# Kernel optimization log

Measured on AMD Instinct MI355X. Metric: run time of the kernel, lower is better.

## Reference

```python
import jax, jax.numpy as jnp
import numpy as np

B, T = 32, 512
DA, DV = 1280, 768
D = DA + DV          # fused audio+video feature dim = 2048
DM = 256             # mamba d_model
L = 4                # n_layers
DI = 2 * DM          # d_inner (expand=2)
DS = 16              # d_state
DC = 4               # d_conv
R = DM // 16         # dt_rank = ceil(256/16)
H = 128              # attn-pool hidden
NC = 8               # emotion classes
EPS_TIN = 1e-5
EPS_LN = 1e-5


def _ln(x, g, b):
    mu = x.mean(-1, keepdims=True)
    v = ((x - mu) ** 2).mean(-1, keepdims=True)
    return (x - mu) / jnp.sqrt(v + EPS_LN) * g + b


def _mamba(u, in_w, cw, cb, xw, dtw, dtb, A_log, Dp, ow):
    # u: [B,T,DM] -> [B,T,DM]; Mamba(v1) selective scan, d_state=16, d_conv=4, expand=2
    xz = jnp.einsum('btd,ed->bte', u, in_w)            # [B,T,2*DI]
    x, z = xz[..., :DI], xz[..., DI:]
    xp = jnp.pad(x, ((0, 0), (DC - 1, 0), (0, 0)))     # causal depthwise conv1d
    xc = sum(xp[:, k:k + u.shape[1], :] * cw[:, k] for k in range(DC)) + cb
    x = jax.nn.silu(xc)
    dbc = jnp.einsum('btd,ed->bte', x, xw)             # [B,T,R+2*DS]
    dt = jax.nn.softplus(jnp.einsum('btr,dr->btd', dbc[..., :R], dtw) + dtb)
    Bm = dbc[..., R:R + DS]
    Cm = dbc[..., R + DS:]
    A = -jnp.exp(A_log)                                # [DI,DS]

    def step(h, inp):
        dt_t, B_t, C_t, x_t = inp                      # [B,DI],[B,DS],[B,DS],[B,DI]
        h = jnp.exp(dt_t[..., None] * A) * h + dt_t[..., None] * B_t[:, None, :] * x_t[..., None]
        return h, jnp.einsum('bds,bs->bd', h, C_t)

    h0 = jnp.zeros((u.shape[0], DI, DS), u.dtype)
    xs = (dt.swapaxes(0, 1), Bm.swapaxes(0, 1), Cm.swapaxes(0, 1), x.swapaxes(0, 1))
    _, ys = jax.lax.scan(step, h0, xs)
    y = ys.swapaxes(0, 1) + Dp * x
    y = y * jax.nn.silu(z)
    return jnp.einsum('bti,oi->bto', y, ow)


def _forward(x, tin_gamma, tin_beta, proj_w, proj_b, ln_g, ln_b, in_proj_w, conv_w, conv_b,
             x_proj_w, dt_proj_w, dt_proj_b, A_log, D_param, out_proj_w,
             out_ln_g, out_ln_b, res_scale, attn_w1, attn_b1, attn_w2, head_w, head_b, lengths):
    mask = jnp.arange(T)[None, :] < lengths[:, None]   # [B,T]
    m = mask[..., None].astype(x.dtype)
    # FusedTIN: masked temporal instance norm + affine
    denom = jnp.maximum(lengths, 1).astype(x.dtype)[:, None, None]
    mean = (x * m).sum(1, keepdims=True) / denom
    var = (((x - mean) ** 2) * m).sum(1, keepdims=True) / denom
    xn = (x - mean) / jnp.sqrt(var + EPS_TIN) * m
    xn = (xn * tin_gamma + tin_beta) * m
    # MambaStack: proj_in + prenorm residual mamba blocks (dropout = eval identity)
    h = jnp.einsum('btd,md->btm', xn, proj_w) + proj_b
    for l in range(L):
        y = _mamba(_ln(h, ln_g[l], ln_b[l]), in_proj_w[l], conv_w[l], conv_b[l],
                   x_proj_w[l], dt_proj_w[l], dt_proj_b[l], A_log[l], D_param[l], out_proj_w[l])
        h = h + res_scale * y
    h = _ln(h, out_ln_g, out_ln_b)
    # MaskedAttnPool
    s = jnp.einsum('bth,oh->bto', jnp.tanh(jnp.einsum('btd,hd->bth', h, attn_w1) + attn_b1), attn_w2)[..., 0]
    logits = jnp.where(mask, s, -jnp.inf)
    alpha = jnp.nan_to_num(jax.nn.softmax(logits, axis=1)) * mask
    alpha = alpha / jnp.clip(alpha.sum(1, keepdims=True), 1e-9)
    ctx = (alpha[..., None] * h).sum(1)
    # classifier head
    return jnp.einsum('bd,cd->bc', ctx, head_w) + head_b


def setup_inputs() -> dict:
    key = jax.random.key(0)
    ks = jax.random.split(key, 16)
    s = 0.05
    inp = {}
    inp['x'] = jax.random.normal(ks[0], (B, T, D), jnp.float32)
    inp['lengths'] = jax.random.randint(ks[1], (B,), T // 4, T + 1)
    inp['tin_gamma'] = jnp.ones((D,), jnp.float32)
    inp['tin_beta'] = jnp.zeros((D,), jnp.float32)
    inp['proj_w'] = jax.random.normal(ks[2], (DM, D), jnp.float32) * s
    inp['proj_b'] = jnp.zeros((DM,), jnp.float32)
    inp['ln_g'] = jnp.ones((L, DM), jnp.float32)
    inp['ln_b'] = jnp.zeros((L, DM), jnp.float32)
    inp['in_proj_w'] = jax.random.normal(ks[3], (L, 2 * DI, DM), jnp.float32) * s
    inp['conv_w'] = jax.random.normal(ks[4], (L, DI, DC), jnp.float32) * s
    inp['conv_b'] = jnp.zeros((L, DI), jnp.float32)
    inp['x_proj_w'] = jax.random.normal(ks[5], (L, R + 2 * DS, DI), jnp.float32) * s
    inp['dt_proj_w'] = jax.random.normal(ks[6], (L, DI, R), jnp.float32) * s
    inp['dt_proj_b'] = jnp.full((L, DI), -3.0, jnp.float32) + jax.random.normal(ks[7], (L, DI), jnp.float32) * 0.1
    inp['A_log'] = jnp.log(jnp.broadcast_to(jnp.arange(1, DS + 1, dtype=jnp.float32), (L, DI, DS)) + 0.0)
    inp['D_param'] = jnp.ones((L, DI), jnp.float32)
    inp['out_proj_w'] = jax.random.normal(ks[8], (L, DM, DI), jnp.float32) * s
    inp['out_ln_g'] = jnp.ones((DM,), jnp.float32)
    inp['out_ln_b'] = jnp.zeros((DM,), jnp.float32)
    inp['res_scale'] = jnp.asarray(0.1, jnp.float32)
    inp['attn_w1'] = jax.random.normal(ks[9], (H, DM), jnp.float32) * s
    inp['attn_b1'] = jnp.zeros((H,), jnp.float32)
    inp['attn_w2'] = jax.random.normal(ks[10], (1, H), jnp.float32) * s
    inp['head_w'] = jax.random.normal(ks[11], (NC, DM), jnp.float32) * s
    inp['head_b'] = jnp.zeros((NC,), jnp.float32)
    return inp


def reference(x, tin_gamma, tin_beta, proj_w, proj_b, ln_g, ln_b, in_proj_w, conv_w, conv_b,
              x_proj_w, dt_proj_w, dt_proj_b, A_log, D_param, out_proj_w,
              out_ln_g, out_ln_b, res_scale, attn_w1, attn_b1, attn_w2, head_w, head_b, lengths):
    return _forward(x, tin_gamma, tin_beta, proj_w, proj_b, ln_g, ln_b, in_proj_w, conv_w, conv_b,
                    x_proj_w, dt_proj_w, dt_proj_b, A_log, D_param, out_proj_w,
                    out_ln_g, out_ln_b, res_scale, attn_w1, attn_b1, attn_w2, head_w, head_b, lengths)
```

## Files before the change

kernel.cpp:

```cpp
#include <hip/hip_runtime.h>

#define NB 32
#define NT 512
#define ND 2048
#define NDM 256
#define NDI 512
#define NDS 16
#define NR 16
#define NDC 4
#define NH 128
#define NNC 8
#define NL 4
#define NM (NB*NT)

typedef __attribute__((ext_vector_type(8))) short short8;
typedef __attribute__((ext_vector_type(4))) float floatx4;

__device__ __forceinline__ unsigned short f2bf_rn(float f) {
    unsigned u = __builtin_bit_cast(unsigned, f);
    u += 0x7FFFu + ((u >> 16) & 1u);
    return (unsigned short)(u >> 16);
}

__global__ __launch_bounds__(256) void tin_stats_k(
    const float* __restrict__ x, const int* __restrict__ lengths,
    float* __restrict__ mean, float* __restrict__ rstd)
{
    __shared__ float rs_[4][64];
    __shared__ float rq_[4][64];
    const int b = blockIdx.x >> 5;
    const int d0 = (blockIdx.x & 31) << 6;
    const int dl = threadIdx.x & 63;
    const int strip = threadIdx.x >> 6;
    const int len = lengths[b];
    const int d = d0 + dl;
    float s = 0.f, q = 0.f;
    for (int t = strip; t < len; t += 4) {
        float v = x[((size_t)(b*NT + t))*ND + d];
        s += v; q += v*v;
    }
    rs_[strip][dl] = s; rq_[strip][dl] = q;
    __syncthreads();
    if (threadIdx.x < 64) {
        float S = rs_[0][dl]+rs_[1][dl]+rs_[2][dl]+rs_[3][dl];
        float Q = rq_[0][dl]+rq_[1][dl]+rq_[2][dl]+rq_[3][dl];
        float inv = 1.f / (float)(len < 1 ? 1 : len);
        float mu = S * inv;
        float var = Q * inv - mu*mu;
        mean[b*ND + d] = mu;
        rstd[b*ND + d] = rsqrtf(var + 1e-5f);
    }
}

#define A_HI 0
#define A_LO 4096
#define B_HI 8192
#define B_LO 12288

template<int AMODE, int EPI>
__global__ __launch_bounds__(256) void mgemm_k(
    const float* __restrict__ A, int lda,
    const float* __restrict__ A2, int lda2,
    const float* __restrict__ W,
    const float* __restrict__ bias,
    float* __restrict__ C,
    int M, int N, int K,
    const float* __restrict__ mean, const float* __restrict__ rstd,
    const float* __restrict__ gamma, const float* __restrict__ beta,
    const int* __restrict__ lengths,
    const float* __restrict__ rsp)
{
    __shared__ __align__(16) short lds[16384];
    const int tid = threadIdx.x;
    const int lane = tid & 63;
    const int w = tid >> 6;
    const int lm = lane & 15;
    const int lc = lane >> 4;
    const int wm = w >> 1;
    const int wn = w & 1;
    const int m0 = blockIdx.x * 128;
    const int n0 = blockIdx.y * 128;

    int lenb = 0, bb = 0;
    if (AMODE == 1) { bb = m0 >> 9; lenb = lengths[bb]; }

    floatx4 acc[4][4];
#pragma unroll
    for (int i = 0; i < 4; ++i)
#pragma unroll
        for (int j = 0; j < 4; ++j) acc[i][j] = (floatx4){0.f,0.f,0.f,0.f};

    for (int k0 = 0; k0 < K; k0 += 32) {
        float va[2][8], vb[2][8];
#pragma unroll
        for (int hh = 0; hh < 2; ++hh) {
            const int mt = w*2 + hh;
            const int gm = m0 + mt*16 + lm;
            const int kg = k0 + lc*8;
            const float* ap = A + (size_t)gm*lda + kg;
            float4 a0 = *(const float4*)ap;
            float4 a1 = *(const float4*)(ap + 4);
            if (AMODE == 1) {
                const int tcur = gm & (NT-1);
                if (tcur >= lenb) {
                    a0 = make_float4(0.f,0.f,0.f,0.f); a1 = a0;
                } else {
                    const int kb = bb*ND + kg;
                    float4 mn0 = *(const float4*)(mean + kb);
                    float4 mn1 = *(const float4*)(mean + kb + 4);
                    float4 rr0 = *(const float4*)(rstd + kb);
                    float4 rr1 = *(const float4*)(rstd + kb + 4);
                    float4 g0 = *(const float4*)(gamma + kg);
                    float4 g1 = *(const float4*)(gamma + kg + 4);
                    float4 e0 = *(const float4*)(beta + kg);
                    float4 e1 = *(const float4*)(beta + kg + 4);
                    a0.x = (a0.x - mn0.x)*rr0.x*g0.x + e0.x;
                    a0.y = (a0.y - mn0.y)*rr0.y*g0.y + e0.y;
                    a0.z = (a0.z - mn0.z)*rr0.z*g0.z + e0.z;
                    a0.w = (a0.w - mn0.w)*rr0.w*g0.w + e0.w;
                    a1.x = (a1.x - mn1.x)*rr1.x*g1.x + e1.x;
                    a1.y = (a1.y - mn1.y)*rr1.y*g1.y + e1.y;
                    a1.z = (a1.z - mn1.z)*rr1.z*g1.z + e1.z;
                    a1.w = (a1.w - mn1.w)*rr1.w*g1.w + e1.w;
                }
            } else if (AMODE == 2) {
                const float* zp = A2 + (size_t)gm*lda2 + kg;
                float4 z0 = *(const float4*)zp;
                float4 z1 = *(const float4*)(zp + 4);
                a0.x *= z0.x / (1.f + __expf(-z0.x));
                a0.y *= z0.y / (1.f + __expf(-z0.y));
                a0.z *= z0.z / (1.f + __expf(-z0.z));
                a0.w *= z0.w / (1.f + __expf(-z0.w));
                a1.x *= z1.x / (1.f + __expf(-z1.x));
                a1.y *= z1.y / (1.f + __expf(-z1.y));
                a1.z *= z1.z / (1.f + __expf(-z1.z));
                a1.w *= z1.w / (1.f + __expf(-z1.w));
            }
            va[hh][0]=a0.x; va[hh][1]=a0.y; va[hh][2]=a0.z; va[hh][3]=a0.w;
            va[hh][4]=a1.x; va[hh][5]=a1.y; va[hh][6]=a1.z; va[hh][7]=a1.w;
        }
#pragma unroll
        for (int hh = 0; hh < 2; ++hh) {
            const int nt = w*2 + hh;
            const int gn = n0 + nt*16 + lm;
            float4 w0, w1;
            if (gn < N) {
                const float* wp = W + (size_t)gn*K + k0 + lc*8;
                w0 = *(const float4*)wp;
                w1 = *(const float4*)(wp + 4);
            } else {
                w0 = make_float4(0.f,0.f,0.f,0.f); w1 = w0;
            }
            vb[hh][0]=w0.x; vb[hh][1]=w0.y; vb[hh][2]=w0.z; vb[hh][3]=w0.w;
            vb[hh][4]=w1.x; vb[hh][5]=w1.y; vb[hh][6]=w1.z; vb[hh][7]=w1.w;
        }
        __syncthreads();
#pragma unroll
        for (int hh = 0; hh < 2; ++hh) {
            short8 h8, l8;
#pragma unroll
            for (int q = 0; q < 8; ++q) {
                unsigned short hb = f2bf_rn(va[hh][q]);
                float hf = __builtin_bit_cast(float, (unsigned)hb << 16);
                h8[q] = (short)hb;
                l8[q] = (short)f2bf_rn(va[hh][q] - hf);
            }
            const int off = ((w*2 + hh)*64 + lane)*8;
            *(short8*)&lds[A_HI + off] = h8;
            *(short8*)&lds[A_LO + off] = l8;
        }
#pragma unroll
        for (int hh = 0; hh < 2; ++hh) {
            short8 h8, l8;
#pragma unroll
            for (int q = 0; q < 8; ++q) {
                unsigned short hb = f2bf_rn(vb[hh][q]);
                float hf = __builtin_bit_cast(float, (unsigned)hb << 16);
                h8[q] = (short)hb;
                l8[q] = (short)f2bf_rn(vb[hh][q] - hf);
            }
            const int off = ((w*2 + hh)*64 + lane)*8;
            *(short8*)&lds[B_HI + off] = h8;
            *(short8*)&lds[B_LO + off] = l8;
        }
        __syncthreads();
        short8 ah[4], al[4], bh[4], bl[4];
#pragma unroll
        for (int i = 0; i < 4; ++i) {
            const int off = ((wm*4 + i)*64 + lane)*8;
            ah[i] = *(const short8*)&lds[A_HI + off];
            al[i] = *(const short8*)&lds[A_LO + off];
        }
#pragma unroll
        for (int j = 0; j < 4; ++j) {
            const int off = ((wn*4 + j)*64 + lane)*8;
            bh[j] = *(const short8*)&lds[B_HI + off];
            bl[j] = *(const short8*)&lds[B_LO + off];
        }
#pragma unroll
        for (int i = 0; i < 4; ++i)
#pragma unroll
            for (int j = 0; j < 4; ++j) {
                acc[i][j] = __builtin_amdgcn_mfma_f32_16x16x32_bf16(ah[i], bh[j], acc[i][j], 0, 0, 0);
                acc[i][j] = __builtin_amdgcn_mfma_f32_16x16x32_bf16(ah[i], bl[j], acc[i][j], 0, 0, 0);
                acc[i][j] = __builtin_amdgcn_mfma_f32_16x16x32_bf16(al[i], bh[j], acc[i][j], 0, 0, 0);
            }
    }

    const float rs = (EPI == 1) ? rsp[0] : 0.f;
#pragma unroll
    for (int j = 0; j < 4; ++j) {
        const int n = n0 + wn*64 + j*16 + lm;
        if (n < N) {
            const float bv = (EPI != 1 && bias) ? bias[n] : 0.f;
#pragma unroll
            for (int i = 0; i < 4; ++i) {
#pragma unroll
                for (int r = 0; r < 4; ++r) {
                    const int m = m0 + wm*64 + i*16 + lc*4 + r;
                    float v = acc[i][j][r];
                    float* cp = C + (size_t)m*N + n;
                    if (EPI == 0)      *cp = v + bv;
                    else if (EPI == 1) *cp = fmaf(rs, v, *cp);
                    else               *cp = tanhf(v + bv);
                }
            }
        }
    }
}

__global__ __launch_bounds__(256) void ln_k(
    const float* __restrict__ in, float* __restrict__ out,
    const float* __restrict__ g, const float* __restrict__ b)
{
    const int w = threadIdx.x >> 6;
    const int lane = threadIdx.x & 63;
    const int m = blockIdx.x*4 + w;
    const float4 v = *(const float4*)(in + (size_t)m*NDM + lane*4);
    float s = v.x+v.y+v.z+v.w;
    float q = v.x*v.x + v.y*v.y + v.z*v.z + v.w*v.w;
#pragma unroll
    for (int o = 32; o; o >>= 1) { s += __shfl_xor(s, o); q += __shfl_xor(q, o); }
    const float mu = s * (1.f/NDM);
    const float var = q * (1.f/NDM) - mu*mu;
    const float r = rsqrtf(var + 1e-5f);
    const float4 g4 = *(const float4*)(g + lane*4);
    const float4 b4 = *(const float4*)(b + lane*4);
    float4 o;
    o.x = (v.x-mu)*r*g4.x + b4.x;
    o.y = (v.y-mu)*r*g4.y + b4.y;
    o.z = (v.z-mu)*r*g4.z + b4.z;
    o.w = (v.w-mu)*r*g4.w + b4.w;
    *(float4*)(out + (size_t)m*NDM + lane*4) = o;
}

__global__ __launch_bounds__(256) void conv_k(
    const float* __restrict__ xz, const float* __restrict__ cw,
    const float* __restrict__ cb, float* __restrict__ xc)
{
    const int m = blockIdx.x >> 1;
    const int i = ((blockIdx.x & 1) << 8) + threadIdx.x;
    const int t = m & (NT-1);
    const float4 w4 = *(const float4*)(cw + i*4);
    const float* base = xz + (size_t)m*(2*NDI) + i;
    float acc = cb[i] + base[0]*w4.w;
    if (t >= 1) acc += base[-(2*NDI)]  * w4.z;
    if (t >= 2) acc += base[-2*(2*NDI)]* w4.y;
    if (t >= 3) acc += base[-3*(2*NDI)]* w4.x;
    xc[(size_t)m*NDI + i] = acc / (1.f + __expf(-acc));
}

#define TCH 64
__global__ __launch_bounds__(256) void scan_k(
    const float* __restrict__ dbc,
    const float* __restrict__ xc,
    const float* __restrict__ dtw,
    const float* __restrict__ dtb,
    const float* __restrict__ Alog,
    const float* __restrict__ Dp,
    float* __restrict__ y)
{
    __shared__ float sR[TCH][16];
    __shared__ float sB[TCH][16];
    __shared__ float sC[TCH][16];
    __shared__ float sX[TCH][16];
    __shared__ float sDT[TCH][16];
    __shared__ float sY[TCH][16];
    const int tid = threadIdx.x;
    const int s = tid & 15;
    const int di = tid >> 4;
    const int b = blockIdx.x >> 5;
    const int d0 = (blockIdx.x & 31) << 4;
    const int d = d0 + di;
    const float Av = -__expf(Alog[d*NDS + s]);
    const float dpv = Dp[d];
    const float dtbd = dtb[d];
    float wrow[16];
#pragma unroll
    for (int r = 0; r < 16; ++r) wrow[r] = dtw[d*NR + r];
    float h = 0.f;
    const int jrow = tid >> 2;
    const int q4 = (tid & 3) << 2;
    const size_t mbase = (size_t)b * NT;
    for (int c0 = 0; c0 < NT; c0 += TCH) {
        __syncthreads();
        {
            const size_t m = mbase + c0 + jrow;
            const float* dp_ = dbc + m*48 + q4;
            *(float4*)&sR[jrow][q4] = *(const float4*)(dp_);
            *(float4*)&sB[jrow][q4] = *(const float4*)(dp_ + 16);
            *(float4*)&sC[jrow][q4] = *(const float4*)(dp_ + 32);
            *(float4*)&sX[jrow][q4] = *(const float4*)(xc + m*NDI + d0 + q4);
        }
        __syncthreads();
#pragma unroll
        for (int u2 = 0; u2 < 4; ++u2) {
            const int j = s + u2*16;
            float a = dtbd;
#pragma unroll
            for (int r = 0; r < 16; ++r) a = fmaf(sR[j][r], wrow[r], a);
            sDT[j][di] = (a > 20.f) ? a : log1pf(__expf(a));
        }
        __syncthreads();
        for (int j = 0; j < TCH; ++j) {
            const float dtv = sDT[j][di];
            const float xv = sX[j][di];
            const float Bv = sB[j][s];
            const float Cv = sC[j][s];
            const float pa = __expf(dtv * Av);
            h = fmaf(pa, h, dtv * Bv * xv);
            float cp = h * Cv;
            cp += __shfl_xor(cp, 1);
            cp += __shfl_xor(cp, 2);
            cp += __shfl_xor(cp, 4);
            cp += __shfl_xor(cp, 8);
            if (s == 0) sY[j][di] = fmaf(dpv, xv, cp);
        }
        __syncthreads();
        {
            const size_t m = mbase + c0 + jrow;
            *(float4*)(y + m*NDI + d0 + q4) = *(const float4*)&sY[jrow][q4];
        }
    }
}

__global__ __launch_bounds__(64) void score_k(
    const float* __restrict__ t1, const float* __restrict__ w2,
    float* __restrict__ sout)
{
    const int m = blockIdx.x;
    const int lane = threadIdx.x;
    float v = t1[(size_t)m*NH + lane]*w2[lane]
            + t1[(size_t)m*NH + 64 + lane]*w2[64 + lane];
#pragma unroll
    for (int o = 32; o; o >>= 1) v += __shfl_xor(v, o);
    if (lane == 0) sout[m] = v;
}

__global__ __launch_bounds__(256) void pool_k(
    const float* __restrict__ sbuf, const float* __restrict__ u,
    const int* __restrict__ lengths, float* __restrict__ ctx)
{
    __shared__ float al[NT];
    __shared__ float red[256];
    const int b = blockIdx.x;
    const int tid = threadIdx.x;
    const int len = lengths[b];
    float mx = -3.4e38f;
    for (int t = tid; t < len; t += 256) mx = fmaxf(mx, sbuf[b*NT + t]);
    red[tid] = mx; __syncthreads();
    for (int o = 128; o; o >>= 1) { if (tid < o) red[tid] = fmaxf(red[tid], red[tid+o]); __syncthreads(); }
    mx = red[0];
    __syncthreads();
    float sm = 0.f;
    for (int t = tid; t < len; t += 256) {
        float e = __expf(sbuf[b*NT + t] - mx);
        al[t] = e; sm += e;
    }
    red[tid] = sm; __syncthreads();
    for (int o = 128; o; o >>= 1) { if (tid < o) red[tid] += red[tid+o]; __syncthreads(); }
    const float rZ = 1.f / red[0];
    float acc = 0.f;
    const float* up = u + (size_t)b*NT*NDM + tid;
    for (int t = 0; t < len; ++t) acc = fmaf(al[t], up[(size_t)t*NDM], acc);
    ctx[b*NDM + tid] = acc * rZ;
}

__global__ __launch_bounds__(64) void head_k(
    const float* __restrict__ ctx, const float* __restrict__ hw,
    const float* __restrict__ hb, float* __restrict__ o)
{
    const int b = blockIdx.x;
    const int lane = threadIdx.x;
    const float4 c4 = *(const float4*)(ctx + b*NDM + lane*4);
#pragma unroll
    for (int c = 0; c < NNC; ++c) {
        const float4 w4 = *(const float4*)(hw + c*NDM + lane*4);
        float v = c4.x*w4.x + c4.y*w4.y + c4.z*w4.z + c4.w*w4.w;
#pragma unroll
        for (int off = 32; off; off >>= 1) v += __shfl_xor(v, off);
        if (lane == 0) o[b*NNC + c] = v + hb[c];
    }
}

extern "C" void kernel_launch(void* const* d_in, const int* in_sizes, int n_in,
                              void* d_out, int out_size, void* d_ws, size_t ws_size,
                              hipStream_t stream)
{
    (void)in_sizes; (void)n_in; (void)out_size; (void)ws_size;
    const float* x         = (const float*)d_in[0];
    const int*   lengths   = (const int*)  d_in[1];
    const float* tin_gamma = (const float*)d_in[2];
    const float* tin_beta  = (const float*)d_in[3];
    const float* proj_w    = (const float*)d_in[4];
    const float* proj_b    = (const float*)d_in[5];
    const float* ln_g      = (const float*)d_in[6];
    const float* ln_b      = (const float*)d_in[7];
    const float* in_proj_w = (const float*)d_in[8];
    const float* conv_w    = (const float*)d_in[9];
    const float* conv_b    = (const float*)d_in[10];
    const float* x_proj_w  = (const float*)d_in[11];
    const float* dt_proj_w = (const float*)d_in[12];
    const float* dt_proj_b = (const float*)d_in[13];
    const float* A_log     = (const float*)d_in[14];
    const float* D_param   = (const float*)d_in[15];
    const float* out_proj_w= (const float*)d_in[16];
    const float* out_ln_g  = (const float*)d_in[17];
    const float* out_ln_b  = (const float*)d_in[18];
    const float* res_scale = (const float*)d_in[19];
    const float* attn_w1   = (const float*)d_in[20];
    const float* attn_b1   = (const float*)d_in[21];
    const float* attn_w2   = (const float*)d_in[22];
    const float* head_w    = (const float*)d_in[23];
    const float* head_b    = (const float*)d_in[24];
    float* out = (float*)d_out;

    float* ws   = (float*)d_ws;
    float* mean = ws;
    float* rstd = mean + (size_t)NB*ND;
    float* hbuf = rstd + (size_t)NB*ND;
    float* ubuf = hbuf + (size_t)NM*NDM;
    float* xz   = ubuf + (size_t)NM*NDM;
    float* xc   = xz   + (size_t)NM*2*NDI;
    float* ybuf = xc   + (size_t)NM*NDI;
    float* dbc  = ybuf + (size_t)NM*NDI;
    float* t1   = dbc  + (size_t)NM*48;
    float* sbuf = t1   + (size_t)NM*NH;
    float* ctx  = sbuf + NM;

    const dim3 blk(256);

    tin_stats_k<<<dim3(NB*32), blk, 0, stream>>>(x, lengths, mean, rstd);
    mgemm_k<1,0><<<dim3(NM/128, NDM/128), blk, 0, stream>>>(
        x, ND, nullptr, 0, proj_w, proj_b, hbuf, NM, NDM, ND,
        mean, rstd, tin_gamma, tin_beta, lengths, nullptr);

    for (int l = 0; l < NL; ++l) {
        ln_k<<<dim3(NM/4), blk, 0, stream>>>(hbuf, ubuf, ln_g + l*NDM, ln_b + l*NDM);
        mgemm_k<0,0><<<dim3(NM/128, (2*NDI)/128), blk, 0, stream>>>(
            ubuf, NDM, nullptr, 0, in_proj_w + (size_t)l*2*NDI*NDM, nullptr,
            xz, NM, 2*NDI, NDM, nullptr, nullptr, nullptr, nullptr, nullptr, nullptr);
        conv_k<<<dim3(NM*2), blk, 0, stream>>>(
            xz, conv_w + (size_t)l*NDI*NDC, conv_b + (size_t)l*NDI, xc);
        mgemm_k<0,0><<<dim3(NM/128, 1), blk, 0, stream>>>(
            xc, NDI, nullptr, 0, x_proj_w + (size_t)l*48*NDI, nullptr,
            dbc, NM, 48, NDI, nullptr, nullptr, nullptr, nullptr, nullptr, nullptr);
        scan_k<<<dim3(NB*32), blk, 0, stream>>>(
            dbc, xc, dt_proj_w + (size_t)l*NDI*NR, dt_proj_b + (size_t)l*NDI,
            A_log + (size_t)l*NDI*NDS, D_param + (size_t)l*NDI, ybuf);
        mgemm_k<2,1><<<dim3(NM/128, NDM/128), blk, 0, stream>>>(
            ybuf, NDI, xz + NDI, 2*NDI, out_proj_w + (size_t)l*NDM*NDI, nullptr,
            hbuf, NM, NDM, NDI, nullptr, nullptr, nullptr, nullptr, nullptr, res_scale);
    }

    ln_k<<<dim3(NM/4), blk, 0, stream>>>(hbuf, ubuf, out_ln_g, out_ln_b);
    mgemm_k<0,2><<<dim3(NM/128, 1), blk, 0, stream>>>(
        ubuf, NDM, nullptr, 0, attn_w1, attn_b1, t1, NM, NH, NDM,
        nullptr, nullptr, nullptr, nullptr, nullptr, nullptr);
    score_k<<<dim3(NM), dim3(64), 0, stream>>>(t1, attn_w2, sbuf);
    pool_k<<<dim3(NB), blk, 0, stream>>>(sbuf, ubuf, lengths, ctx);
    head_k<<<dim3(NB), dim3(64), 0, stream>>>(ctx, head_w, head_b, out);
}
```

Baseline: 1.865 ms.

## Pre-split operands into blocked bf16 hi/lo tiles and restructure Mamba pipeline

Producers (TIN norm, layernorm, conv, scan) now write activations directly as pre-split bf16 hi/lo pairs in an MFMA-fragment-blocked layout, and weights are converted once per call by a new wconv kernel. The GEMM becomes a templated kernel with configurable tile sizes that streams pre-converted fragments with register prefetch instead of doing fp32 loads and conversion inside the K loop. The dt projection is split out into its own kernel, the scan is reworked to cover more channels per block and fuse the SiLU(z) gating plus hi/lo conversion, and conv and layernorm are blocked to match. This removes repeated fp32-to-bf16 splitting and fused prologue math from the GEMM inner loops. In exchange it adds extra kernels, extra intermediate buffers and more memory traffic for the split activations.

```diff
diff --git a/kernel.cpp b/kernel.cpp
--- a/kernel.cpp
+++ b/kernel.cpp
@@ -7,7 +7,6 @@
 #define NDI 512
 #define NDS 16
 #define NR 16
-#define NDC 4
 #define NH 128
 #define NNC 8
 #define NL 4
@@ -20,6 +19,15 @@
     unsigned u = __builtin_bit_cast(unsigned, f);
     u += 0x7FFFu + ((u >> 16) & 1u);
     return (unsigned short)(u >> 16);
+}
+__device__ __forceinline__ void cvt8(const float* v, short8& h8, short8& l8) {
+#pragma unroll
+    for (int q = 0; q < 8; ++q) {
+        unsigned short hb = f2bf_rn(v[q]);
+        float hf = __builtin_bit_cast(float, (unsigned)hb << 16);
+        h8[q] = (short)hb;
+        l8[q] = (short)f2bf_rn(v[q] - hf);
+    }
 }
 
 __global__ __launch_bounds__(256) void tin_stats_k(
@@ -52,174 +60,189 @@
     }
 }
 
-#define A_HI 0
-#define A_LO 4096
-#define B_HI 8192
-#define B_LO 12288
-
-template<int AMODE, int EPI>
+#define SLN 264
+__global__ __launch_bounds__(256) void tin_norm_k(
+    const float* __restrict__ x, const int* __restrict__ lengths,
+    const float* __restrict__ mean, const float* __restrict__ rstd,
+    const float* __restrict__ g, const float* __restrict__ be,
+    short* __restrict__ Oh, short* __restrict__ Ol)
+{
+    __shared__ float sT[16][SLN];
+    const int tid = threadIdx.x;
+    const int row = tid >> 4, c = tid & 15;
+    const int m = blockIdx.x*16 + row;
+    const int b = m >> 9, t = m & (NT-1);
+    const int len = lengths[b];
+    const int kg0 = blockIdx.y*256 + c*16;
+    if (t >= len) {
+#pragma unroll
+        for (int i = 0; i < 16; ++i) sT[row][c*16 + i] = 0.f;
+    } else {
+#pragma unroll
+        for (int qq = 0; qq < 4; ++qq) {
+            const int kg = kg0 + qq*4;
+            float4 v = *(const float4*)(x + (size_t)m*ND + kg);
+            float4 mn = *(const float4*)(mean + b*ND + kg);
+            float4 rr = *(const float4*)(rstd + b*ND + kg);
+            float4 gg = *(const float4*)(g + kg);
+            float4 bb = *(const float4*)(be + kg);
+            sT[row][c*16+qq*4+0] = (v.x-mn.x)*rr.x*gg.x + bb.x;
+            sT[row][c*16+qq*4+1] = (v.y-mn.y)*rr.y*gg.y + bb.y;
+            sT[row][c*16+qq*4+2] = (v.z-mn.z)*rr.z*gg.z + bb.z;
+            sT[row][c*16+qq*4+3] = (v.w-mn.w)*rr.w*gg.w + bb.w;
+        }
+    }
+    __syncthreads();
+#pragma unroll
+    for (int q = 0; q < 2; ++q) {
+        const int slot = tid + 256*q;
+        const int tile = slot >> 6, ln2 = slot & 63;
+        const int mr = ln2 & 15, kc = ln2 >> 4;
+        float v[8];
+        *(float4*)&v[0] = *(const float4*)&sT[mr][tile*32 + kc*8];
+        *(float4*)&v[4] = *(const float4*)&sT[mr][tile*32 + kc*8 + 4];
+        short8 h8, l8; cvt8(v, h8, l8);
+        const size_t off = ((size_t)blockIdx.x*64 + blockIdx.y*8 + tile)*512 + ln2*8;
+        *(short8*)(Oh + off) = h8;
+        *(short8*)(Ol + off) = l8;
+    }
+}
+
+__global__ __launch_bounds__(256) void wconv_k(
+    const float* __restrict__ W, short* __restrict__ Oh, short* __restrict__ Ol,
+    int K, int nmod, int nvalid)
+{
+    __shared__ float sT[16][SLN];
+    const int tid = threadIdx.x;
+    const int row = tid >> 4, c = tid & 15;
+    const int n = blockIdx.x*16 + row;
+    const int rr = n % nmod;
+    const int kg0 = blockIdx.y*256 + c*16;
+    if (rr >= nvalid) {
+#pragma unroll
+        for (int i = 0; i < 16; ++i) sT[row][c*16 + i] = 0.f;
+    } else {
+        const int src = (n/nmod)*nvalid + rr;
+#pragma unroll
+        for (int qq = 0; qq < 4; ++qq) {
+            float4 v = *(const float4*)(W + (size_t)src*K + kg0 + qq*4);
+            *(float4*)&sT[row][c*16+qq*4] = v;
+        }
+    }
+    __syncthreads();
+#pragma unroll
+    for (int q = 0; q < 2; ++q) {
+        const int slot = tid + 256*q;
+        const int tile = slot >> 6, ln2 = slot & 63;
+        const int mr = ln2 & 15, kc = ln2 >> 4;
+        float v[8];
+        *(float4*)&v[0] = *(const float4*)&sT[mr][tile*32 + kc*8];
+        *(float4*)&v[4] = *(const float4*)&sT[mr][tile*32 + kc*8 + 4];
+        short8 h8, l8; cvt8(v, h8, l8);
+        const size_t off = ((size_t)blockIdx.x*(K>>5) + blockIdx.y*8 + tile)*512 + ln2*8;
+        *(short8*)(Oh + off) = h8;
+        *(short8*)(Ol + off) = l8;
+    }
+}
+
+template<int MSUB, int NSUB, int EPI>
 __global__ __launch_bounds__(256) void mgemm_k(
-    const float* __restrict__ A, int lda,
-    const float* __restrict__ A2, int lda2,
-    const float* __restrict__ W,
-    const float* __restrict__ bias,
-    float* __restrict__ C,
-    int M, int N, int K,
-    const float* __restrict__ mean, const float* __restrict__ rstd,
-    const float* __restrict__ gamma, const float* __restrict__ beta,
-    const int* __restrict__ lengths,
-    const float* __restrict__ rsp)
-{
-    __shared__ __align__(16) short lds[16384];
-    const int tid = threadIdx.x;
-    const int lane = tid & 63;
-    const int w = tid >> 6;
-    const int lm = lane & 15;
-    const int lc = lane >> 4;
-    const int wm = w >> 1;
-    const int wn = w & 1;
-    const int m0 = blockIdx.x * 128;
-    const int n0 = blockIdx.y * 128;
-
-    int lenb = 0, bb = 0;
-    if (AMODE == 1) { bb = m0 >> 9; lenb = lengths[bb]; }
-
-    floatx4 acc[4][4];
-#pragma unroll
-    for (int i = 0; i < 4; ++i)
-#pragma unroll
-        for (int j = 0; j < 4; ++j) acc[i][j] = (floatx4){0.f,0.f,0.f,0.f};
-
-    for (int k0 = 0; k0 < K; k0 += 32) {
-        float va[2][8], vb[2][8];
-#pragma unroll
-        for (int hh = 0; hh < 2; ++hh) {
-            const int mt = w*2 + hh;
-            const int gm = m0 + mt*16 + lm;
-            const int kg = k0 + lc*8;
-            const float* ap = A + (size_t)gm*lda + kg;
-            float4 a0 = *(const float4*)ap;
-            float4 a1 = *(const float4*)(ap + 4);
-            if (AMODE == 1) {
-                const int tcur = gm & (NT-1);
-                if (tcur >= lenb) {
-                    a0 = make_float4(0.f,0.f,0.f,0.f); a1 = a0;
-                } else {
-                    const int kb = bb*ND + kg;
-                    float4 mn0 = *(const float4*)(mean + kb);
-                    float4 mn1 = *(const float4*)(mean + kb + 4);
-                    float4 rr0 = *(const float4*)(rstd + kb);
-                    float4 rr1 = *(const float4*)(rstd + kb + 4);
-                    float4 g0 = *(const float4*)(gamma + kg);
-                    float4 g1 = *(const float4*)(gamma + kg + 4);
-                    float4 e0 = *(const float4*)(beta + kg);
-                    float4 e1 = *(const float4*)(beta + kg + 4);
-                    a0.x = (a0.x - mn0.x)*rr0.x*g0.x + e0.x;
-                    a0.y = (a0.y - mn0.y)*rr0.y*g0.y + e0.y;
-                    a0.z = (a0.z - mn0.z)*rr0.z*g0.z + e0.z;
-                    a0.w = (a0.w - mn0.w)*rr0.w*g0.w + e0.w;
-                    a1.x = (a1.x - mn1.x)*rr1.x*g1.x + e1.x;
-                    a1.y = (a1.y - mn1.y)*rr1.y*g1.y + e1.y;
-                    a1.z = (a1.z - mn1.z)*rr1.z*g1.z + e1.z;
-                    a1.w = (a1.w - mn1.w)*rr1.w*g1.w + e1.w;
-                }
-            } else if (AMODE == 2) {
-                const float* zp = A2 + (size_t)gm*lda2 + kg;
-                float4 z0 = *(const float4*)zp;
-                float4 z1 = *(const float4*)(zp + 4);
-                a0.x *= z0.x / (1.f + __expf(-z0.x));
-                a0.y *= z0.y / (1.f + __expf(-z0.y));
-                a0.z *= z0.z / (1.f + __expf(-z0.z));
-                a0.w *= z0.w / (1.f + __expf(-z0.w));
-                a1.x *= z1.x / (1.f + __expf(-z1.x));
-                a1.y *= z1.y / (1.f + __expf(-z1.y));
-                a1.z *= z1.z / (1.f + __expf(-z1.z));
-                a1.w *= z1.w / (1.f + __expf(-z1.w));
+    const short* __restrict__ Ah, const short* __restrict__ Al,
+    const short* __restrict__ Bh, const short* __restrict__ Bl,
+    const float* __restrict__ bias, float* __restrict__ C,
+    int ldc, int Nvalid, int K, const float* __restrict__ rsp)
+{
+    __shared__ __align__(16) short lds[(MSUB+NSUB)*1024];
+    short* As_h = lds;
+    short* As_l = lds + MSUB*512;
+    short* Bs_h = lds + MSUB*1024;
+    short* Bs_l = lds + MSUB*1024 + NSUB*512;
+    const int tid = threadIdx.x, lane = tid & 63, w = tid >> 6;
+    const int m0t = blockIdx.x * MSUB;
+    const int n0t = blockIdx.y * NSUB;
+    const int Ktiles = K >> 5;
+    constexpr int MI = MSUB/2, NI = NSUB/2;
+    constexpr int ASG = MSUB/4, BSG = NSUB/4;
+    const int wm = w >> 1, wn = w & 1;
+
+    floatx4 acc[MI][NI] = {};
+    short8 rah[ASG], ral[ASG], rbh[BSG], rbl[BSG];
+
+#pragma unroll
+    for (int u = 0; u < ASG; ++u) {
+        const size_t off = ((size_t)(m0t + w*ASG + u)*Ktiles)*512 + lane*8;
+        rah[u] = *(const short8*)(Ah + off); ral[u] = *(const short8*)(Al + off);
+    }
+#pragma unroll
+    for (int u = 0; u < BSG; ++u) {
+        const size_t off = ((size_t)(n0t + w*BSG + u)*Ktiles)*512 + lane*8;
+        rbh[u] = *(const short8*)(Bh + off); rbl[u] = *(const short8*)(Bl + off);
+    }
+
+    for (int kb = 0; kb < Ktiles; ++kb) {
+        __syncthreads();
+#pragma unroll
+        for (int u = 0; u < ASG; ++u) {
+            const int sub = w*ASG + u;
+            *(short8*)&As_h[sub*512 + lane*8] = rah[u];
+            *(short8*)&As_l[sub*512 + lane*8] = ral[u];
+        }
+#pragma unroll
+        for (int u = 0; u < BSG; ++u) {
+            const int sub = w*BSG + u;
+            *(short8*)&Bs_h[sub*512 + lane*8] = rbh[u];
+            *(short8*)&Bs_l[sub*512 + lane*8] = rbl[u];
+        }
+        __syncthreads();
+        if (kb + 1 < Ktiles) {
+#pragma unroll
+            for (int u = 0; u < ASG; ++u) {
+                const size_t off = ((size_t)(m0t + w*ASG + u)*Ktiles + kb + 1)*512 + lane*8;
+                rah[u] = *(const short8*)(Ah + off); ral[u] = *(const short8*)(Al + off);
             }
-            va[hh][0]=a0.x; va[hh][1]=a0.y; va[hh][2]=a0.z; va[hh][3]=a0.w;
-            va[hh][4]=a1.x; va[hh][5]=a1.y; va[hh][6]=a1.z; va[hh][7]=a1.w;
-        }
-#pragma unroll
-        for (int hh = 0; hh < 2; ++hh) {
-            const int nt = w*2 + hh;
-            const int gn = n0 + nt*16 + lm;
-            float4 w0, w1;
-            if (gn < N) {
-                const float* wp = W + (size_t)gn*K + k0 + lc*8;
-                w0 = *(const float4*)wp;
-                w1 = *(const float4*)(wp + 4);
-            } else {
-                w0 = make_float4(0.f,0.f,0.f,0.f); w1 = w0;
+#pragma unroll
+            for (int u = 0; u < BSG; ++u) {
+                const size_t off = ((size_t)(n0t + w*BSG + u)*Ktiles + kb + 1)*512 + lane*8;
+                rbh[u] = *(const short8*)(Bh + off); rbl[u] = *(const short8*)(Bl + off);
             }
-            vb[hh][0]=w0.x; vb[hh][1]=w0.y; vb[hh][2]=w0.z; vb[hh][3]=w0.w;
-            vb[hh][4]=w1.x; vb[hh][5]=w1.y; vb[hh][6]=w1.z; vb[hh][7]=w1.w;
-        }
-        __syncthreads();
-#pragma unroll
-        for (int hh = 0; hh < 2; ++hh) {
-            short8 h8, l8;
-#pragma unroll
-            for (int q = 0; q < 8; ++q) {
-                unsigned short hb = f2bf_rn(va[hh][q]);
-                float hf = __builtin_bit_cast(float, (unsigned)hb << 16);
-                h8[q] = (short)hb;
-                l8[q] = (short)f2bf_rn(va[hh][q] - hf);
+        }
+        short8 fah[MI], fal[MI], fbh[NI], fbl[NI];
+#pragma unroll
+        for (int i = 0; i < MI; ++i) {
+            const int sub = wm*MI + i;
+            fah[i] = *(const short8*)&As_h[sub*512 + lane*8];
+            fal[i] = *(const short8*)&As_l[sub*512 + lane*8];
+        }
+#pragma unroll
+        for (int j = 0; j < NI; ++j) {
+            const int sub = wn*NI + j;
+            fbh[j] = *(const short8*)&Bs_h[sub*512 + lane*8];
+            fbl[j] = *(const short8*)&Bs_l[sub*512 + lane*8];
+        }
+#pragma unroll
+        for (int i = 0; i < MI; ++i)
+#pragma unroll
+            for (int j = 0; j < NI; ++j) {
+                acc[i][j] = __builtin_amdgcn_mfma_f32_16x16x32_bf16(fah[i], fbh[j], acc[i][j], 0, 0, 0);
+                acc[i][j] = __builtin_amdgcn_mfma_f32_16x16x32_bf16(fah[i], fbl[j], acc[i][j], 0, 0, 0);
+                acc[i][j] = __builtin_amdgcn_mfma_f32_16x16x32_bf16(fal[i], fbh[j], acc[i][j], 0, 0, 0);
             }
-            const int off = ((w*2 + hh)*64 + lane)*8;
-            *(short8*)&lds[A_HI + off] = h8;
-            *(short8*)&lds[A_LO + off] = l8;
-        }
-#pragma unroll
-        for (int hh = 0; hh < 2; ++hh) {
-            short8 h8, l8;
-#pragma unroll
-            for (int q = 0; q < 8; ++q) {
-                unsigned short hb = f2bf_rn(vb[hh][q]);
-                float hf = __builtin_bit_cast(float, (unsigned)hb << 16);
-                h8[q] = (short)hb;
-                l8[q] = (short)f2bf_rn(vb[hh][q] - hf);
-            }
-            const int off = ((w*2 + hh)*64 + lane)*8;
-            *(short8*)&lds[B_HI + off] = h8;
-            *(short8*)&lds[B_LO + off] = l8;
-        }
-        __syncthreads();
-        short8 ah[4], al[4], bh[4], bl[4];
-#pragma unroll
-        for (int i = 0; i < 4; ++i) {
-            const int off = ((wm*4 + i)*64 + lane)*8;
-            ah[i] = *(const short8*)&lds[A_HI + off];
-            al[i] = *(const short8*)&lds[A_LO + off];
-        }
-#pragma unroll
-        for (int j = 0; j < 4; ++j) {
-            const int off = ((wn*4 + j)*64 + lane)*8;
-            bh[j] = *(const short8*)&lds[B_HI + off];
-            bl[j] = *(const short8*)&lds[B_LO + off];
-        }
-#pragma unroll
-        for (int i = 0; i < 4; ++i)
-#pragma unroll
-            for (int j = 0; j < 4; ++j) {
-                acc[i][j] = __builtin_amdgcn_mfma_f32_16x16x32_bf16(ah[i], bh[j], acc[i][j], 0, 0, 0);
-                acc[i][j] = __builtin_amdgcn_mfma_f32_16x16x32_bf16(ah[i], bl[j], acc[i][j], 0, 0, 0);
-                acc[i][j] = __builtin_amdgcn_mfma_f32_16x16x32_bf16(al[i], bh[j], acc[i][j], 0, 0, 0);
-            }
     }
 
     const float rs = (EPI == 1) ? rsp[0] : 0.f;
-#pragma unroll
-    for (int j = 0; j < 4; ++j) {
-        const int n = n0 + wn*64 + j*16 + lm;
-        if (n < N) {
+    const int lc = lane >> 4, col = lane & 15;
+#pragma unroll
+    for (int j = 0; j < NI; ++j) {
+        const int n = (n0t + wn*NI + j)*16 + col;
+        if (n < Nvalid) {
             const float bv = (EPI != 1 && bias) ? bias[n] : 0.f;
 #pragma unroll
-            for (int i = 0; i < 4; ++i) {
+            for (int i = 0; i < MI; ++i) {
+                const int mb = (m0t + wm*MI + i)*16 + lc*4;
 #pragma unroll
                 for (int r = 0; r < 4; ++r) {
-                    const int m = m0 + wm*64 + i*16 + lc*4 + r;
                     float v = acc[i][j][r];
-                    float* cp = C + (size_t)m*N + n;
+                    float* cp = C + (size_t)(mb + r)*ldc + n;
                     if (EPI == 0)      *cp = v + bv;
                     else if (EPI == 1) *cp = fmaf(rs, v, *cp);
                     else               *cp = tanhf(v + bv);
@@ -229,118 +252,231 @@
     }
 }
 
-__global__ __launch_bounds__(256) void ln_k(
-    const float* __restrict__ in, float* __restrict__ out,
-    const float* __restrict__ g, const float* __restrict__ b)
-{
-    const int w = threadIdx.x >> 6;
-    const int lane = threadIdx.x & 63;
-    const int m = blockIdx.x*4 + w;
-    const float4 v = *(const float4*)(in + (size_t)m*NDM + lane*4);
-    float s = v.x+v.y+v.z+v.w;
-    float q = v.x*v.x + v.y*v.y + v.z*v.z + v.w*v.w;
-#pragma unroll
-    for (int o = 32; o; o >>= 1) { s += __shfl_xor(s, o); q += __shfl_xor(q, o); }
+template<int WF32>
+__global__ __launch_bounds__(256) void ln_blk_k(
+    const float* __restrict__ in, const float* __restrict__ g,
+    const float* __restrict__ b,
+    short* __restrict__ Oh, short* __restrict__ Ol, float* __restrict__ o32)
+{
+    __shared__ float sT[16][SLN];
+    const int tid = threadIdx.x;
+    const int row = tid >> 4, c = tid & 15;
+    const int m = blockIdx.x*16 + row;
+    float v[16];
+#pragma unroll
+    for (int qq = 0; qq < 4; ++qq)
+        *(float4*)&v[qq*4] = *(const float4*)(in + (size_t)m*NDM + c*16 + qq*4);
+    float s = 0.f, q = 0.f;
+#pragma unroll
+    for (int i = 0; i < 16; ++i) { s += v[i]; q += v[i]*v[i]; }
+#pragma unroll
+    for (int o = 8; o; o >>= 1) { s += __shfl_xor(s, o); q += __shfl_xor(q, o); }
     const float mu = s * (1.f/NDM);
-    const float var = q * (1.f/NDM) - mu*mu;
-    const float r = rsqrtf(var + 1e-5f);
-    const float4 g4 = *(const float4*)(g + lane*4);
-    const float4 b4 = *(const float4*)(b + lane*4);
-    float4 o;
-    o.x = (v.x-mu)*r*g4.x + b4.x;
-    o.y = (v.y-mu)*r*g4.y + b4.y;
-    o.z = (v.z-mu)*r*g4.z + b4.z;
-    o.w = (v.w-mu)*r*g4.w + b4.w;
-    *(float4*)(out + (size_t)m*NDM + lane*4) = o;
-}
-
-__global__ __launch_bounds__(256) void conv_k(
+    const float r = rsqrtf(q*(1.f/NDM) - mu*mu + 1e-5f);
+#pragma unroll
+    for (int i = 0; i < 16; ++i) {
+        const int kg = c*16 + i;
+        v[i] = (v[i]-mu)*r*g[kg] + b[kg];
+        sT[row][kg] = v[i];
+    }
+    if (WF32) {
+#pragma unroll
+        for (int qq = 0; qq < 4; ++qq)
+            *(float4*)(o32 + (size_t)m*NDM + c*16 + qq*4) = *(const float4*)&v[qq*4];
+    }
+    __syncthreads();
+#pragma unroll
+    for (int qv = 0; qv < 2; ++qv) {
+        const int slot = tid + 256*qv;
+        const int tile = slot >> 6, ln2 = slot & 63;
+        const int mr = ln2 & 15, kc = ln2 >> 4;
+        float vv[8];
+        *(float4*)&vv[0] = *(const float4*)&sT[mr][tile*32 + kc*8];
+        *(float4*)&vv[4] = *(const float4*)&sT[mr][tile*32 + kc*8 + 4];
+        short8 h8, l8; cvt8(vv, h8, l8);
+        const size_t off = ((size_t)blockIdx.x*8 + tile)*512 + ln2*8;
+        *(short8*)(Oh + off) = h8;
+        *(short8*)(Ol + off) = l8;
+    }
+}
+
+#define SCV 520
+__global__ __launch_bounds__(256) void conv_blk_k(
     const float* __restrict__ xz, const float* __restrict__ cw,
-    const float* __restrict__ cb, float* __restrict__ xc)
-{
-    const int m = blockIdx.x >> 1;
-    const int i = ((blockIdx.x & 1) << 8) + threadIdx.x;
+    const float* __restrict__ cb, float* __restrict__ xc32,
+    short* __restrict__ Oh, short* __restrict__ Ol)
+{
+    __shared__ float sT[16][SCV];
+    const int tid = threadIdx.x;
+    const int row = tid >> 4, cg = tid & 15;
+    const int m = blockIdx.x*16 + row;
     const int t = m & (NT-1);
-    const float4 w4 = *(const float4*)(cw + i*4);
-    const float* base = xz + (size_t)m*(2*NDI) + i;
-    float acc = cb[i] + base[0]*w4.w;
-    if (t >= 1) acc += base[-(2*NDI)]  * w4.z;
-    if (t >= 2) acc += base[-2*(2*NDI)]* w4.y;
-    if (t >= 3) acc += base[-3*(2*NDI)]* w4.x;
-    xc[(size_t)m*NDI + i] = acc / (1.f + __expf(-acc));
-}
-
-#define TCH 64
+#pragma unroll
+    for (int grp = 0; grp < 4; ++grp) {
+        const int ch = cg*32 + grp*8;
+        float a[8];
+        *(float4*)&a[0] = *(const float4*)(cb + ch);
+        *(float4*)&a[4] = *(const float4*)(cb + ch + 4);
+        float4 wv[8];
+#pragma unroll
+        for (int i = 0; i < 8; ++i) wv[i] = *(const float4*)(cw + (ch+i)*4);
+#pragma unroll
+        for (int kk = 0; kk < 4; ++kk) {
+            if (t - 3 + kk >= 0) {
+                const float* xp = xz + (size_t)(m-3+kk)*(2*NDI) + ch;
+                float xv[8];
+                *(float4*)&xv[0] = *(const float4*)xp;
+                *(float4*)&xv[4] = *(const float4*)(xp + 4);
+                const float tap[8] = {
+                    kk==0?wv[0].x:kk==1?wv[0].y:kk==2?wv[0].z:wv[0].w,
+                    kk==0?wv[1].x:kk==1?wv[1].y:kk==2?wv[1].z:wv[1].w,
+                    kk==0?wv[2].x:kk==1?wv[2].y:kk==2?wv[2].z:wv[2].w,
+                    kk==0?wv[3].x:kk==1?wv[3].y:kk==2?wv[3].z:wv[3].w,
+                    kk==0?wv[4].x:kk==1?wv[4].y:kk==2?wv[4].z:wv[4].w,
+                    kk==0?wv[5].x:kk==1?wv[5].y:kk==2?wv[5].z:wv[5].w,
+                    kk==0?wv[6].x:kk==1?wv[6].y:kk==2?wv[6].z:wv[6].w,
+                    kk==0?wv[7].x:kk==1?wv[7].y:kk==2?wv[7].z:wv[7].w};
+#pragma unroll
+                for (int i = 0; i < 8; ++i) a[i] = fmaf(xv[i], tap[i], a[i]);
+            }
+        }
+#pragma unroll
+        for (int i = 0; i < 8; ++i) a[i] = a[i] / (1.f + __expf(-a[i]));
+        *(float4*)&sT[row][ch] = *(const float4*)&a[0];
+        *(float4*)&sT[row][ch+4] = *(const float4*)&a[4];
+        *(float4*)(xc32 + (size_t)m*NDI + ch) = *(const float4*)&a[0];
+        *(float4*)(xc32 + (size_t)m*NDI + ch + 4) = *(const float4*)&a[4];
+    }
+    __syncthreads();
+#pragma unroll
+    for (int q = 0; q < 4; ++q) {
+        const int slot = tid + 256*q;
+        const int tile = slot >> 6, ln2 = slot & 63;
+        const int mr = ln2 & 15, kc = ln2 >> 4;
+        float vv[8];
+        *(float4*)&vv[0] = *(const float4*)&sT[mr][tile*32 + kc*8];
+        *(float4*)&vv[4] = *(const float4*)&sT[mr][tile*32 + kc*8 + 4];
+        short8 h8, l8; cvt8(vv, h8, l8);
+        const size_t off = ((size_t)blockIdx.x*16 + tile)*512 + ln2*8;
+        *(short8*)(Oh + off) = h8;
+        *(short8*)(Ol + off) = l8;
+    }
+}
+
+__global__ __launch_bounds__(256) void dt_k(
+    const float* __restrict__ dbc, const float* __restrict__ dtw,
+    const float* __restrict__ dtb, float* __restrict__ dt)
+{
+    const int m = blockIdx.x;
+    const float* rsrc = dbc + (size_t)m*48;
+    float rv[16];
+#pragma unroll
+    for (int i = 0; i < 16; ++i) rv[i] = rsrc[i];
+#pragma unroll
+    for (int hh = 0; hh < 2; ++hh) {
+        const int d = hh*256 + threadIdx.x;
+        const float* wr = dtw + d*16;
+        float a = dtb[d];
+#pragma unroll
+        for (int i = 0; i < 16; ++i) a = fmaf(rv[i], wr[i], a);
+        dt[(size_t)m*NDI + d] = (a > 20.f) ? a : log1pf(__expf(a));
+    }
+}
+
 __global__ __launch_bounds__(256) void scan_k(
-    const float* __restrict__ dbc,
-    const float* __restrict__ xc,
-    const float* __restrict__ dtw,
-    const float* __restrict__ dtb,
-    const float* __restrict__ Alog,
-    const float* __restrict__ Dp,
-    float* __restrict__ y)
-{
-    __shared__ float sR[TCH][16];
-    __shared__ float sB[TCH][16];
-    __shared__ float sC[TCH][16];
-    __shared__ float sX[TCH][16];
-    __shared__ float sDT[TCH][16];
-    __shared__ float sY[TCH][16];
+    const float* __restrict__ dbc, const float* __restrict__ dtp,
+    const float* __restrict__ xcp, const float* __restrict__ xz,
+    const float* __restrict__ Alog, const float* __restrict__ Dp,
+    short* __restrict__ Yh, short* __restrict__ Yl)
+{
+    __shared__ float sBC[64][32];
+    __shared__ float sY[64][68];
     const int tid = threadIdx.x;
-    const int s = tid & 15;
-    const int di = tid >> 4;
-    const int b = blockIdx.x >> 5;
-    const int d0 = (blockIdx.x & 31) << 4;
-    const int d = d0 + di;
-    const float Av = -__expf(Alog[d*NDS + s]);
-    const float dpv = Dp[d];
-    const float dtbd = dtb[d];
-    float wrow[16];
-#pragma unroll
-    for (int r = 0; r < 16; ++r) wrow[r] = dtw[d*NR + r];
-    float h = 0.f;
-    const int jrow = tid >> 2;
-    const int q4 = (tid & 3) << 2;
-    const size_t mbase = (size_t)b * NT;
-    for (int c0 = 0; c0 < NT; c0 += TCH) {
+    const int w = tid >> 6, lane = tid & 63;
+    const int dl = lane >> 2, sg = lane & 3;
+    const int b = blockIdx.x >> 3;
+    const int d0 = (blockIdx.x & 7) << 6;
+    const int dloc = w*16 + dl;
+    const int d = d0 + dloc;
+    float ar[4];
+    {
+        float4 al4 = *(const float4*)(Alog + d*NDS + sg*4);
+        ar[0] = -__expf(al4.x); ar[1] = -__expf(al4.y);
+        ar[2] = -__expf(al4.z); ar[3] = -__expf(al4.w);
+    }
+    const float Dpv = Dp[d];
+    float hr[4] = {0.f, 0.f, 0.f, 0.f};
+    const int mbase = b*NT;
+    const int srow = tid >> 2, sq = (tid & 3) << 3;
+
+    for (int c0 = 0; c0 < NT; c0 += 64) {
+        {
+            const float* dp_ = dbc + (size_t)(mbase + c0 + srow)*48 + 16 + sq;
+            *(float4*)&sBC[srow][sq]   = *(const float4*)dp_;
+            *(float4*)&sBC[srow][sq+4] = *(const float4*)(dp_ + 4);
+        }
         __syncthreads();
-        {
-            const size_t m = mbase + c0 + jrow;
-            const float* dp_ = dbc + m*48 + q4;
-            *(float4*)&sR[jrow][q4] = *(const float4*)(dp_);
-            *(float4*)&sB[jrow][q4] = *(const float4*)(dp_ + 16);
-            *(float4*)&sC[jrow][q4] = *(const float4*)(dp_ + 32);
-            *(float4*)&sX[jrow][q4] = *(const float4*)(xc + m*NDI + d0 + q4);
+        float pdt[2][4], px[2][4];
+#pragma unroll
+        for (int u = 0; u < 4; ++u) {
+            const size_t mm = (size_t)(mbase + c0 + u);
+            pdt[0][u] = dtp[mm*NDI + d];
+            px[0][u]  = xcp[mm*NDI + d];
+        }
+#pragma unroll
+        for (int tg = 0; tg < 16; ++tg) {
+            const int cur = tg & 1, nxt = cur ^ 1;
+            if (tg < 15) {
+#pragma unroll
+                for (int u = 0; u < 4; ++u) {
+                    const size_t mm = (size_t)(mbase + c0 + (tg+1)*4 + u);
+                    pdt[nxt][u] = dtp[mm*NDI + d];
+                    px[nxt][u]  = xcp[mm*NDI + d];
+                }
+            }
+#pragma unroll
+            for (int u = 0; u < 4; ++u) {
+                const int tloc = tg*4 + u;
+                const float dtv = pdt[cur][u], xv = px[cur][u];
+                const float4 Bv = *(const float4*)&sBC[tloc][sg*4];
+                const float4 Cv = *(const float4*)&sBC[tloc][16 + sg*4];
+                const float dbx = dtv * xv;
+                float cp;
+                {
+                    float pa = __expf(dtv*ar[0]); hr[0] = fmaf(pa, hr[0], dbx*Bv.x); cp = hr[0]*Cv.x;
+                    pa = __expf(dtv*ar[1]); hr[1] = fmaf(pa, hr[1], dbx*Bv.y); cp = fmaf(hr[1], Cv.y, cp);
+                    pa = __expf(dtv*ar[2]); hr[2] = fmaf(pa, hr[2], dbx*Bv.z); cp = fmaf(hr[2], Cv.z, cp);
+                    pa = __expf(dtv*ar[3]); hr[3] = fmaf(pa, hr[3], dbx*Bv.w); cp = fmaf(hr[3], Cv.w, cp);
+                }
+                cp += __shfl_xor(cp, 1);
+                cp += __shfl_xor(cp, 2);
+                if (sg == 0) sY[tloc][dloc] = fmaf(Dpv, xv, cp);
+            }
         }
         __syncthreads();
 #pragma unroll
-        for (int u2 = 0; u2 < 4; ++u2) {
-            const int j = s + u2*16;
-            float a = dtbd;
-#pragma unroll
-            for (int r = 0; r < 16; ++r) a = fmaf(sR[j][r], wrow[r], a);
-            sDT[j][di] = (a > 20.f) ? a : log1pf(__expf(a));
+        for (int q = 0; q < 2; ++q) {
+            const int slot = tid + 256*q;
+            const int tile = slot >> 6, ln2 = slot & 63;
+            const int tm = tile >> 1, tk = tile & 1;
+            const int mr = ln2 & 15, kc = ln2 >> 4;
+            const int m = mbase + c0 + tm*16 + mr;
+            const int kd = d0 + tk*32 + kc*8;
+            float yv[8];
+            *(float4*)&yv[0] = *(const float4*)&sY[tm*16 + mr][tk*32 + kc*8];
+            *(float4*)&yv[4] = *(const float4*)&sY[tm*16 + mr][tk*32 + kc*8 + 4];
+            float zv[8];
+            *(float4*)&zv[0] = *(const float4*)(xz + (size_t)m*(2*NDI) + NDI + kd);
+            *(float4*)&zv[4] = *(const float4*)(xz + (size_t)m*(2*NDI) + NDI + kd + 4);
+#pragma unroll
+            for (int i = 0; i < 8; ++i)
+                yv[i] *= zv[i] / (1.f + __expf(-zv[i]));
+            short8 h8, l8; cvt8(yv, h8, l8);
+            const size_t off = ((size_t)(m>>4)*16 + (kd>>5))*512 + ln2*8;
+            *(short8*)(Yh + off) = h8;
+            *(short8*)(Yl + off) = l8;
         }
         __syncthreads();
-        for (int j = 0; j < TCH; ++j) {
-            const float dtv = sDT[j][di];
-            const float xv = sX[j][di];
-            const float Bv = sB[j][s];
-            const float Cv = sC[j][s];
-            const float pa = __expf(dtv * Av);
-            h = fmaf(pa, h, dtv * Bv * xv);
-            float cp = h * Cv;
-            cp += __shfl_xor(cp, 1);
-            cp += __shfl_xor(cp, 2);
-            cp += __shfl_xor(cp, 4);
-            cp += __shfl_xor(cp, 8);
-            if (s == 0) sY[j][di] = fmaf(dpv, xv, cp);
-        }
-        __syncthreads();
-        {
-            const size_t m = mbase + c0 + jrow;
-            *(float4*)(y + m*NDI + d0 + q4) = *(const float4*)&sY[jrow][q4];
-        }
     }
 }
 
@@ -435,49 +571,79 @@
     const float* head_b    = (const float*)d_in[24];
     float* out = (float*)d_out;
 
-    float* ws   = (float*)d_ws;
-    float* mean = ws;
-    float* rstd = mean + (size_t)NB*ND;
-    float* hbuf = rstd + (size_t)NB*ND;
-    float* ubuf = hbuf + (size_t)NM*NDM;
-    float* xz   = ubuf + (size_t)NM*NDM;
-    float* xc   = xz   + (size_t)NM*2*NDI;
-    float* ybuf = xc   + (size_t)NM*NDI;
-    float* dbc  = ybuf + (size_t)NM*NDI;
-    float* t1   = dbc  + (size_t)NM*48;
-    float* sbuf = t1   + (size_t)NM*NH;
-    float* ctx  = sbuf + NM;
+    float* ws = (float*)d_ws;
+    float* mean   = ws;
+    float* rstd   = mean + 65536;
+    float* hbuf   = rstd + 65536;
+    float* ubuf32 = hbuf + (size_t)NM*NDM;
+    float* dbc    = ubuf32 + (size_t)NM*NDM;
+    float* t1     = dbc + (size_t)NM*48;
+    float* sbuf   = t1 + (size_t)NM*NH;
+    float* ctx    = sbuf + NM;
+    float* fend   = ctx + NB*NDM;
+    short* ublk_h = (short*)fend;
+    short* ublk_l = ublk_h + (size_t)NM*NDM;
+    short* xcb_h  = ublk_l + (size_t)NM*NDM;
+    short* xcb_l  = xcb_h + (size_t)NM*NDI;
+    short* yq_h   = xcb_l + (size_t)NM*NDI;
+    short* yq_l   = yq_h + (size_t)NM*NDI;
+    short* pw_h   = yq_l + (size_t)NM*NDI;
+    short* pw_l   = pw_h + (size_t)256*2048;
+    short* iw_h   = pw_l + (size_t)256*2048;
+    short* iw_l   = iw_h + (size_t)4*1024*256;
+    short* xw_h   = iw_l + (size_t)4*1024*256;
+    short* xw_l   = xw_h + (size_t)4*64*512;
+    short* ow_h   = xw_l + (size_t)4*64*512;
+    short* ow_l   = ow_h + (size_t)4*256*512;
+    short* aw_h   = ow_l + (size_t)4*256*512;
+    short* aw_l   = aw_h + (size_t)128*256;
+    float* over   = (float*)(aw_l + (size_t)128*256);
+    short* xn_h   = (short*)over;
+    short* xn_l   = xn_h + (size_t)NM*ND;
+    float* xz     = over;
+    float* xc32   = over + (size_t)NM*2*NDI;
+    float* dtb_   = xc32 + (size_t)NM*NDI;
 
     const dim3 blk(256);
 
+    wconv_k<<<dim3(16, 8), blk, 0, stream>>>(proj_w, pw_h, pw_l, 2048, 1<<28, 1<<28);
+    wconv_k<<<dim3(256, 1), blk, 0, stream>>>(in_proj_w, iw_h, iw_l, 256, 1<<28, 1<<28);
+    wconv_k<<<dim3(16, 2), blk, 0, stream>>>(x_proj_w, xw_h, xw_l, 512, 64, 48);
+    wconv_k<<<dim3(64, 2), blk, 0, stream>>>(out_proj_w, ow_h, ow_l, 512, 1<<28, 1<<28);
+    wconv_k<<<dim3(8, 1), blk, 0, stream>>>(attn_w1, aw_h, aw_l, 256, 1<<28, 1<<28);
+
     tin_stats_k<<<dim3(NB*32), blk, 0, stream>>>(x, lengths, mean, rstd);
-    mgemm_k<1,0><<<dim3(NM/128, NDM/128), blk, 0, stream>>>(
-        x, ND, nullptr, 0, proj_w, proj_b, hbuf, NM, NDM, ND,
-        mean, rstd, tin_gamma, tin_beta, lengths, nullptr);
+    tin_norm_k<<<dim3(NM/16, 8), blk, 0, stream>>>(x, lengths, mean, rstd,
+        tin_gamma, tin_beta, xn_h, xn_l);
+    mgemm_k<4,8,0><<<dim3(256, 2), blk, 0, stream>>>(
+        xn_h, xn_l, pw_h, pw_l, proj_b, hbuf, NDM, NDM, 2048, nullptr);
 
     for (int l = 0; l < NL; ++l) {
-        ln_k<<<dim3(NM/4), blk, 0, stream>>>(hbuf, ubuf, ln_g + l*NDM, ln_b + l*NDM);
-        mgemm_k<0,0><<<dim3(NM/128, (2*NDI)/128), blk, 0, stream>>>(
-            ubuf, NDM, nullptr, 0, in_proj_w + (size_t)l*2*NDI*NDM, nullptr,
-            xz, NM, 2*NDI, NDM, nullptr, nullptr, nullptr, nullptr, nullptr, nullptr);
-        conv_k<<<dim3(NM*2), blk, 0, stream>>>(
-            xz, conv_w + (size_t)l*NDI*NDC, conv_b + (size_t)l*NDI, xc);
-        mgemm_k<0,0><<<dim3(NM/128, 1), blk, 0, stream>>>(
-            xc, NDI, nullptr, 0, x_proj_w + (size_t)l*48*NDI, nullptr,
-            dbc, NM, 48, NDI, nullptr, nullptr, nullptr, nullptr, nullptr, nullptr);
-        scan_k<<<dim3(NB*32), blk, 0, stream>>>(
-            dbc, xc, dt_proj_w + (size_t)l*NDI*NR, dt_proj_b + (size_t)l*NDI,
-            A_log + (size_t)l*NDI*NDS, D_param + (size_t)l*NDI, ybuf);
-        mgemm_k<2,1><<<dim3(NM/128, NDM/128), blk, 0, stream>>>(
-            ybuf, NDI, xz + NDI, 2*NDI, out_proj_w + (size_t)l*NDM*NDI, nullptr,
-            hbuf, NM, NDM, NDI, nullptr, nullptr, nullptr, nullptr, nullptr, res_scale);
-    }
-
-    ln_k<<<dim3(NM/4), blk, 0, stream>>>(hbuf, ubuf, out_ln_g, out_ln_b);
-    mgemm_k<0,2><<<dim3(NM/128, 1), blk, 0, stream>>>(
-        ubuf, NDM, nullptr, 0, attn_w1, attn_b1, t1, NM, NH, NDM,
-        nullptr, nullptr, nullptr, nullptr, nullptr, nullptr);
+        ln_blk_k<0><<<dim3(NM/16), blk, 0, stream>>>(
+            hbuf, ln_g + l*NDM, ln_b + l*NDM, ublk_h, ublk_l, nullptr);
+        mgemm_k<8,8,0><<<dim3(128, 8), blk, 0, stream>>>(
+            ublk_h, ublk_l, iw_h + (size_t)l*1024*256, iw_l + (size_t)l*1024*256,
+            nullptr, xz, 2*NDI, 2*NDI, NDM, nullptr);
+        conv_blk_k<<<dim3(NM/16), blk, 0, stream>>>(
+            xz, conv_w + (size_t)l*NDI*4, conv_b + (size_t)l*NDI, xc32, xcb_h, xcb_l);
+        mgemm_k<4,4,0><<<dim3(256, 1), blk, 0, stream>>>(
+            xcb_h, xcb_l, xw_h + (size_t)l*64*512, xw_l + (size_t)l*64*512,
+            nullptr, dbc, 48, 48, 512, nullptr);
+        dt_k<<<dim3(NM), blk, 0, stream>>>(
+            dbc, dt_proj_w + (size_t)l*NDI*NR, dt_proj_b + (size_t)l*NDI, dtb_);
+        scan_k<<<dim3(NB*8), blk, 0, stream>>>(
+            dbc, dtb_, xc32, xz, A_log + (size_t)l*NDI*NDS, D_param + (size_t)l*NDI,
+            yq_h, yq_l);
+        mgemm_k<4,8,1><<<dim3(256, 2), blk, 0, stream>>>(
+            yq_h, yq_l, ow_h + (size_t)l*256*512, ow_l + (size_t)l*256*512,
+            nullptr, hbuf, NDM, NDM, 512, res_scale);
+    }
+
+    ln_blk_k<1><<<dim3(NM/16), blk, 0, stream>>>(
+        hbuf, out_ln_g, out_ln_b, ublk_h, ublk_l, ubuf32);
+    mgemm_k<4,8,2><<<dim3(256, 1), blk, 0, stream>>>(
+        ublk_h, ublk_l, aw_h, aw_l, attn_b1, t1, NH, NH, 256, nullptr);
     score_k<<<dim3(NM), dim3(64), 0, stream>>>(t1, attn_w2, sbuf);
-    pool_k<<<dim3(NB), blk, 0, stream>>>(sbuf, ubuf, lengths, ctx);
+    pool_k<<<dim3(NB), blk, 0, stream>>>(sbuf, ubuf32, lengths, ctx);
     head_k<<<dim3(NB), dim3(64), 0, stream>>>(ctx, head_w, head_b, out);
 }
```

Result: faster. 1.644 ms (-11.8%).
